# Kernel optimization log

Measured on AMD Instinct MI355X. Metric: run time of the kernel, lower is better.

The kernel has to match this reference:

```python
import jax, jax.numpy as jnp
import numpy as np
from functools import partial

B, H, W, C = 16, 64, 64, 512      # images, feature H, feature W, channels
R = 256                            # raw RPN proposals per image (sorted by objectness)
N_REGIONS = 64                     # regions kept after NMS
PH, PW = 7, 7                      # pool_size (h, w)
IOU_THR = 0.4
FH, FW = H, W                      # feature_size (h, w)
NEG = -jnp.inf


def _nms_indices(roi):
    # roi: [R, 4] (x, y, w, h). Scores are descending by construction
    # (tf.reverse(tf.range(n)/n)), so greedy NMS processes rows in order.
    x, y, w, h = roi[:, 0], roi[:, 1], roi[:, 2], roi[:, 3]
    y1, x1, y2, x2 = y, x, y + h, x + w
    area = (y2 - y1) * (x2 - x1)
    ih = jnp.maximum(jnp.minimum(y2[:, None], y2[None, :]) - jnp.maximum(y1[:, None], y1[None, :]), 0.0)
    iw = jnp.maximum(jnp.minimum(x2[:, None], x2[None, :]) - jnp.maximum(x1[:, None], x1[None, :]), 0.0)
    inter = ih * iw
    union = area[:, None] + area[None, :] - inter
    iou = jnp.where(union > 0, inter / union, 0.0)  # [R, R]

    def step(keep, xs):
        i, row = xs
        suppressed = jnp.any(keep & (row > IOU_THR))
        return keep.at[i].set(~suppressed), None

    keep, _ = jax.lax.scan(step, jnp.zeros((R,), bool), (jnp.arange(R), iou))
    rank = jnp.cumsum(keep.astype(jnp.int32)) - 1
    valid = keep & (rank < N_REGIONS)
    # Unfilled slot j gets tail index R - N_REGIONS + j, which is exactly
    # tf.concat([nms, tf.range(n_roi)[size(nms) - n_regions:]], 0).
    fill = R - N_REGIONS + jnp.arange(N_REGIONS)
    idx = fill.at[jnp.where(valid, rank, N_REGIONS)].set(jnp.arange(R), mode='drop')
    return idx


def _fix_axis(mn, mx, ps, fs):
    pad = ps - (mx - mn)
    fix_min = mn < pad // 2
    fix_max = fs - mx < (1 + pad) // 2
    symmetric = (pad > 0) & ~(fix_min | fix_max)
    omin = jnp.where(symmetric, mn - pad // 2, mn)
    omax = jnp.where(symmetric, mx + (1 + pad) // 2, mx)
    omin = jnp.where((pad > 0) & fix_min, 0, omin)
    omax = jnp.where((pad > 0) & fix_min, ps, omax)
    omin = jnp.where((pad > 0) & fix_max, fs - ps, omin)
    omax = jnp.where((pad > 0) & fix_max, fs, omax)
    return omin, omax


def _clip_roi(roi):
    # roi: [B, N_REGIONS, 4] float (x, y, w, h) -> int32 clipped (x, y, w, h)
    x_min = jnp.maximum(0.0, roi[..., 0]).astype(jnp.int32)
    y_min = jnp.maximum(0.0, roi[..., 1]).astype(jnp.int32)
    x_max = jnp.minimum(float(FW), roi[..., 0] + roi[..., 2]).astype(jnp.int32)
    y_max = jnp.minimum(float(FH), roi[..., 1] + roi[..., 3]).astype(jnp.int32)
    x_min, x_max = _fix_axis(x_min, x_max, PW, FW)   # x axis uses si=1 (width)
    y_min, y_max = _fix_axis(y_min, y_max, PH, FH)   # y axis uses si=0 (height)
    return jnp.stack([x_min, y_min, x_max - x_min, y_max - y_min], axis=-1)


def _pool_one(fm, r):
    # fm: [H, W, C]; r: int32 (x, y, w, h).
    # Faithful to the traced tf.function behaviour of _pool_roi: region.shape[0]
    # is dynamic (None) so region_shape = pool_size, hence h_step = w_step = 1:
    # bins i < PH-1 are single rows y+i; the last bin spans rows [y+PH-1, y+h).
    x, y, w, h = r[0], r[1], r[2], r[3]
    ii = y + jnp.arange(PH - 1)
    jj = x + jnp.arange(PW - 1)
    rmask = (jnp.arange(H) >= y + PH - 1) & (jnp.arange(H) < y + h)
    cmask = (jnp.arange(W) >= x + PW - 1) & (jnp.arange(W) < x + w)
    block = fm[ii[:, None], jj[None, :], :]                                   # [PH-1, PW-1, C]
    col_strip = jnp.max(jnp.where(cmask[None, :, None], fm, NEG), axis=1)     # [H, C]
    corner = jnp.max(jnp.where(rmask[:, None], col_strip, NEG), axis=0)       # [C]
    row_strip = jnp.max(jnp.where(rmask[:, None, None], fm[:, jj, :], NEG), axis=0)  # [PW-1, C]
    top = jnp.concatenate([block, col_strip[ii][:, None, :]], axis=1)         # [PH-1, PW, C]
    bottom = jnp.concatenate([row_strip, corner[None, :]], axis=0)[None]      # [1, PW, C]
    return jnp.concatenate([top, bottom], axis=0)                             # [PH, PW, C]


def _forward(features, roi):
    idx = jax.vmap(_nms_indices)(roi)                           # [B, N_REGIONS]
    roi_nms = jnp.take_along_axis(roi, idx[..., None], axis=1)  # [B, N_REGIONS, 4]
    roi_clipped = _clip_roi(roi_nms)                            # int32 [B, N_REGIONS, 4]
    pooled = jax.vmap(lambda fm, rs: jax.vmap(partial(_pool_one, fm))(rs))(features, roi_clipped)
    return pooled, roi_clipped


def setup_inputs():
    key = jax.random.key(0)
    k1, k2, k3 = jax.random.split(key, 3)
    features = jax.random.normal(k1, (B, H, W, C), dtype=jnp.float32)
    xy = jax.random.uniform(k2, (B, R, 2), dtype=jnp.float32) * 60.0
    wh = jax.random.uniform(k3, (B, R, 2), dtype=jnp.float32) * 30.0 + 2.0
    roi = jnp.concatenate([xy, wh], axis=-1)
    return {"features": features, "roi": roi}


def reference(features, roi):
    return _forward(features, roi)
```

## Files before the change

kernel.cpp:

```cpp
#include <hip/hip_runtime.h>
#include <math.h>

namespace {
constexpr int kB = 16, kH = 64, kW = 64, kC = 512;
constexpr int kR = 256, kN = 64, kPH = 7, kPW = 7;
constexpr int kC4 = kC / 4;
constexpr float kIouThr = 0.4f;
constexpr size_t kPooledElems = (size_t)kB * kN * kPH * kPW * kC;
}

__device__ __forceinline__ float4 max4(float4 a, float4 b) {
    return make_float4(fmaxf(a.x, b.x), fmaxf(a.y, b.y),
                       fmaxf(a.z, b.z), fmaxf(a.w, b.w));
}

__global__ __launch_bounds__(256) void nms_clip_kernel(
        const float* __restrict__ roi, float* __restrict__ out_roi) {
    const int b = blockIdx.x;
    const int tid = threadIdx.x;
    const float* r = roi + (size_t)b * kR * 4;

    __shared__ float4 box[kR];
    __shared__ float area[kR];
    __shared__ unsigned long long M[kR][4];
    __shared__ unsigned long long kw[4];
    __shared__ int idx[kN];

    if (tid < kN) idx[tid] = kR - kN + tid;

    const float4 rr = ((const float4*)r)[tid];
    const float x1 = rr.x, y1 = rr.y, x2 = rr.x + rr.z, y2 = rr.y + rr.w;
    box[tid] = make_float4(x1, y1, x2, y2);
    area[tid] = (y2 - y1) * (x2 - x1);
    __syncthreads();

    {
        unsigned long long m0 = 0, m1 = 0, m2 = 0, m3 = 0;
        const float ai = area[tid];
        for (int j = 0; j < kR; ++j) {
            const float4 bj = box[j];
            const float ih = fmaxf(fminf(y2, bj.w) - fmaxf(y1, bj.y), 0.0f);
            const float iw = fmaxf(fminf(x2, bj.z) - fmaxf(x1, bj.x), 0.0f);
            const float inter = ih * iw;
            const float uni = ai + area[j] - inter;
            const float iou = (uni > 0.0f) ? (inter / uni) : 0.0f;
            if (iou > kIouThr) {
                const unsigned long long bit = 1ull << (j & 63);
                if ((j >> 6) == 0) m0 |= bit;
                else if ((j >> 6) == 1) m1 |= bit;
                else if ((j >> 6) == 2) m2 |= bit;
                else m3 |= bit;
            }
        }
        M[tid][0] = m0; M[tid][1] = m1; M[tid][2] = m2; M[tid][3] = m3;
    }
    __syncthreads();

    if (tid == 0) {
        unsigned long long s0 = 0, s1 = 0, s2 = 0, s3 = 0;
        unsigned long long k0 = 0, k1 = 0, k2 = 0, k3 = 0;
        unsigned long long n0 = M[0][0], n1 = M[0][1], n2 = M[0][2], n3 = M[0][3];
#pragma unroll
        for (int wi = 0; wi < 4; ++wi) {
            for (int bi = 0; bi < 64; ++bi) {
                const unsigned long long m0 = n0, m1 = n1, m2 = n2, m3 = n3;
                const int ip = (wi * 64 + bi + 1) & 255;
                n0 = M[ip][0]; n1 = M[ip][1]; n2 = M[ip][2]; n3 = M[ip][3];
                const unsigned long long sw =
                    (wi == 0) ? s0 : (wi == 1) ? s1 : (wi == 2) ? s2 : s3;
                if (!((sw >> bi) & 1ull)) {
                    const unsigned long long bit = 1ull << bi;
                    if (wi == 0) k0 |= bit;
                    else if (wi == 1) k1 |= bit;
                    else if (wi == 2) k2 |= bit;
                    else k3 |= bit;
                    s0 |= m0; s1 |= m1; s2 |= m2; s3 |= m3;
                }
            }
        }
        kw[0] = k0; kw[1] = k1; kw[2] = k2; kw[3] = k3;
    }
    __syncthreads();

    {
        const int wi = tid >> 6, bi = tid & 63;
        const unsigned long long kwv = kw[wi];
        if ((kwv >> bi) & 1ull) {
            int rank = 0;
            for (int w2 = 0; w2 < wi; ++w2) rank += __popcll(kw[w2]);
            const unsigned long long below =
                (bi == 0) ? 0ull : (~0ull >> (64 - bi));
            rank += __popcll(kwv & below);
            if (rank < kN) idx[rank] = tid;
        }
    }
    __syncthreads();

    if (tid < kN) {
        const int i = idx[tid];
        const float x = r[i * 4 + 0], y = r[i * 4 + 1];
        const float w = r[i * 4 + 2], h = r[i * 4 + 3];
        int x_min = (int)fmaxf(0.0f, x);
        int y_min = (int)fmaxf(0.0f, y);
        int x_max = (int)fminf((float)kW, x + w);
        int y_max = (int)fminf((float)kH, y + h);
        {
            const int pad = kPW - (x_max - x_min);
            const bool fmn = x_min < (pad >> 1);
            const bool fmx = (kW - x_max) < ((1 + pad) >> 1);
            const bool sym = (pad > 0) && !(fmn || fmx);
            int omin = sym ? (x_min - (pad >> 1)) : x_min;
            int omax = sym ? (x_max + ((1 + pad) >> 1)) : x_max;
            if ((pad > 0) && fmn) { omin = 0; omax = kPW; }
            if ((pad > 0) && fmx) { omin = kW - kPW; omax = kW; }
            x_min = omin; x_max = omax;
        }
        {
            const int pad = kPH - (y_max - y_min);
            const bool fmn = y_min < (pad >> 1);
            const bool fmx = (kH - y_max) < ((1 + pad) >> 1);
            const bool sym = (pad > 0) && !(fmn || fmx);
            int omin = sym ? (y_min - (pad >> 1)) : y_min;
            int omax = sym ? (y_max + ((1 + pad) >> 1)) : y_max;
            if ((pad > 0) && fmn) { omin = 0; omax = kPH; }
            if ((pad > 0) && fmx) { omin = kH - kPH; omax = kH; }
            y_min = omin; y_max = omax;
        }
        float4 rf;
        rf.x = (float)x_min; rf.y = (float)y_min;
        rf.z = (float)(x_max - x_min); rf.w = (float)(y_max - y_min);
        ((float4*)out_roi)[b * kN + tid] = rf;
    }
}

__global__ __launch_bounds__(512) void pool_kernel(
        const float4* __restrict__ fm4, const float4* __restrict__ rcf,
        float4* __restrict__ out4) {
    const int rid = blockIdx.x;
    const int b = rid >> 6;
    const int tid = threadIdx.x;
    const int s = tid >> 7;
    const int t = tid & 127;
    const float4 rf = rcf[rid];
    const int x = (int)rf.x, y = (int)rf.y;
    const int w = (int)rf.z, h = (int)rf.w;

    const float4* fm = fm4 + (size_t)b * kH * kW * kC4;
    float4* out = out4 + (size_t)rid * (kPH * kPW) * kC4;

    const float NI = -__builtin_inff();
    const float4 ninf = make_float4(NI, NI, NI, NI);

    for (int p = s; p < 6; p += 4) {
        const float4* row = fm + (size_t)(y + p) * kW * kC4 + t;
#pragma unroll
        for (int q = 0; q < 6; ++q) {
            out[(p * 7 + q) * kC4 + t] = row[(size_t)(x + q) * kC4];
        }
        float4 m = ninf;
        for (int j = x + 6; j < x + w; ++j) {
            m = max4(m, row[(size_t)j * kC4]);
        }
        out[(p * 7 + 6) * kC4 + t] = m;
    }

    float4 pm[7];
#pragma unroll
    for (int o = 0; o < 7; ++o) pm[o] = ninf;
    for (int i = y + 6 + s; i < y + h; i += 4) {
        const float4* row = fm + (size_t)i * kW * kC4 + t;
#pragma unroll
        for (int q = 0; q < 6; ++q) {
            pm[q] = max4(pm[q], row[(size_t)(x + q) * kC4]);
        }
        float4 c = pm[6];
        for (int j = x + 6; j < x + w; ++j) {
            c = max4(c, row[(size_t)j * kC4]);
        }
        pm[6] = c;
    }

    __shared__ float4 red[3][7][128];
    if (s > 0) {
#pragma unroll
        for (int o = 0; o < 7; ++o) red[s - 1][o][t] = pm[o];
    }
    __syncthreads();
    if (s == 0) {
#pragma unroll
        for (int o = 0; o < 7; ++o) {
            float4 v = pm[o];
            v = max4(v, red[0][o][t]);
            v = max4(v, red[1][o][t]);
            v = max4(v, red[2][o][t]);
            out[(42 + o) * kC4 + t] = v;
        }
    }
}

extern "C" void kernel_launch(void* const* d_in, const int* in_sizes, int n_in,
                              void* d_out, int out_size, void* d_ws, size_t ws_size,
                              hipStream_t stream) {
    (void)in_sizes; (void)n_in; (void)d_ws; (void)ws_size; (void)out_size;
    const float* features = (const float*)d_in[0];
    const float* roi = (const float*)d_in[1];
    float* out = (float*)d_out;
    float* out_roi = out + kPooledElems;

    nms_clip_kernel<<<kB, 256, 0, stream>>>(roi, out_roi);
    pool_kernel<<<kB * kN, 512, 0, stream>>>(
        (const float4*)features, (const float4*)out_roi, (float4*)out);
}
```

Before: 346.5 us.

## Split pooling across channel halves, use nontemporal stores, and skip suppressed boxes in NMS

The pooling kernel now launches twice as many 256-thread blocks, each handling half of the channels for one region. Block order is interleaved so that consecutive blocks come from different images. Output writes use nontemporal stores to reduce cache pollution, and the cross-wave reduction becomes a two-stage tree. The serial greedy NMS scan now jumps straight to the next unsuppressed box with ffs instead of testing all 256 bits, which shortens the single-thread critical path at the cost of dependent shared-memory loads.

```diff
diff --git a/kernel.cpp b/kernel.cpp
--- a/kernel.cpp
+++ b/kernel.cpp
@@ -9,9 +9,16 @@
 constexpr size_t kPooledElems = (size_t)kB * kN * kPH * kPW * kC;
 }
 
+typedef float vfloat4 __attribute__((ext_vector_type(4)));
+
 __device__ __forceinline__ float4 max4(float4 a, float4 b) {
     return make_float4(fmaxf(a.x, b.x), fmaxf(a.y, b.y),
                        fmaxf(a.z, b.z), fmaxf(a.w, b.w));
+}
+
+__device__ __forceinline__ void nt_store4(float4* p, float4 v) {
+    vfloat4 nv = { v.x, v.y, v.z, v.w };
+    __builtin_nontemporal_store(nv, (vfloat4*)p);
 }
 
 __global__ __launch_bounds__(256) void nms_clip_kernel(
@@ -59,23 +66,21 @@
     if (tid == 0) {
         unsigned long long s0 = 0, s1 = 0, s2 = 0, s3 = 0;
         unsigned long long k0 = 0, k1 = 0, k2 = 0, k3 = 0;
-        unsigned long long n0 = M[0][0], n1 = M[0][1], n2 = M[0][2], n3 = M[0][3];
 #pragma unroll
         for (int wi = 0; wi < 4; ++wi) {
-            for (int bi = 0; bi < 64; ++bi) {
-                const unsigned long long m0 = n0, m1 = n1, m2 = n2, m3 = n3;
-                const int ip = (wi * 64 + bi + 1) & 255;
-                n0 = M[ip][0]; n1 = M[ip][1]; n2 = M[ip][2]; n3 = M[ip][3];
-                const unsigned long long sw =
-                    (wi == 0) ? s0 : (wi == 1) ? s1 : (wi == 2) ? s2 : s3;
-                if (!((sw >> bi) & 1ull)) {
-                    const unsigned long long bit = 1ull << bi;
-                    if (wi == 0) k0 |= bit;
-                    else if (wi == 1) k1 |= bit;
-                    else if (wi == 2) k2 |= bit;
-                    else k3 |= bit;
-                    s0 |= m0; s1 |= m1; s2 |= m2; s3 |= m3;
-                }
+            unsigned long long* sw =
+                (wi == 0) ? &s0 : (wi == 1) ? &s1 : (wi == 2) ? &s2 : &s3;
+            unsigned long long avail = ~(*sw);
+            while (avail) {
+                const int bi = __ffsll(avail) - 1;
+                const int i = wi * 64 + bi;
+                const unsigned long long bit = 1ull << bi;
+                if (wi == 0) k0 |= bit;
+                else if (wi == 1) k1 |= bit;
+                else if (wi == 2) k2 |= bit;
+                else k3 |= bit;
+                s0 |= M[i][0]; s1 |= M[i][1]; s2 |= M[i][2]; s3 |= M[i][3];
+                avail = ~(*sw) & ~((bit << 1) - 1);
             }
         }
         kw[0] = k0; kw[1] = k1; kw[2] = k2; kw[3] = k3;
@@ -133,14 +138,20 @@
     }
 }
 
-__global__ __launch_bounds__(512) void pool_kernel(
+__global__ __launch_bounds__(256) void pool_kernel(
         const float4* __restrict__ fm4, const float4* __restrict__ rcf,
         float4* __restrict__ out4) {
-    const int rid = blockIdx.x;
-    const int b = rid >> 6;
+    const int bid = blockIdx.x;
+    const int b = bid & 15;
+    const int rest = bid >> 4;
+    const int n = rest & 63;
+    const int ch = rest >> 6;
+    const int rid = b * 64 + n;
     const int tid = threadIdx.x;
-    const int s = tid >> 7;
-    const int t = tid & 127;
+    const int s = tid >> 6;
+    const int t = tid & 63;
+    const int c = ch * 64 + t;
+
     const float4 rf = rcf[rid];
     const int x = (int)rf.x, y = (int)rf.y;
     const int w = (int)rf.z, h = (int)rf.w;
@@ -152,48 +163,55 @@
     const float4 ninf = make_float4(NI, NI, NI, NI);
 
     for (int p = s; p < 6; p += 4) {
-        const float4* row = fm + (size_t)(y + p) * kW * kC4 + t;
+        const float4* row = fm + (size_t)(y + p) * kW * kC4 + c;
 #pragma unroll
         for (int q = 0; q < 6; ++q) {
-            out[(p * 7 + q) * kC4 + t] = row[(size_t)(x + q) * kC4];
+            nt_store4(&out[(p * 7 + q) * kC4 + c], row[(size_t)(x + q) * kC4]);
         }
         float4 m = ninf;
         for (int j = x + 6; j < x + w; ++j) {
             m = max4(m, row[(size_t)j * kC4]);
         }
-        out[(p * 7 + 6) * kC4 + t] = m;
+        nt_store4(&out[(p * 7 + 6) * kC4 + c], m);
     }
 
     float4 pm[7];
 #pragma unroll
     for (int o = 0; o < 7; ++o) pm[o] = ninf;
     for (int i = y + 6 + s; i < y + h; i += 4) {
-        const float4* row = fm + (size_t)i * kW * kC4 + t;
+        const float4* row = fm + (size_t)i * kW * kC4 + c;
 #pragma unroll
         for (int q = 0; q < 6; ++q) {
             pm[q] = max4(pm[q], row[(size_t)(x + q) * kC4]);
         }
-        float4 c = pm[6];
+        float4 cmax = pm[6];
         for (int j = x + 6; j < x + w; ++j) {
-            c = max4(c, row[(size_t)j * kC4]);
-        }
-        pm[6] = c;
-    }
-
-    __shared__ float4 red[3][7][128];
-    if (s > 0) {
-#pragma unroll
-        for (int o = 0; o < 7; ++o) red[s - 1][o][t] = pm[o];
+            cmax = max4(cmax, row[(size_t)j * kC4]);
+        }
+        pm[6] = cmax;
+    }
+
+    __shared__ float4 red[2][7][64];
+    if (s >= 2) {
+#pragma unroll
+        for (int o = 0; o < 7; ++o) red[s - 2][o][t] = pm[o];
+    }
+    __syncthreads();
+    if (s < 2) {
+#pragma unroll
+        for (int o = 0; o < 7; ++o) pm[o] = max4(pm[o], red[s][o][t]);
+    }
+    __syncthreads();
+    if (s == 1) {
+#pragma unroll
+        for (int o = 0; o < 7; ++o) red[0][o][t] = pm[o];
     }
     __syncthreads();
     if (s == 0) {
 #pragma unroll
         for (int o = 0; o < 7; ++o) {
-            float4 v = pm[o];
-            v = max4(v, red[0][o][t]);
-            v = max4(v, red[1][o][t]);
-            v = max4(v, red[2][o][t]);
-            out[(42 + o) * kC4 + t] = v;
+            const float4 v = max4(pm[o], red[0][o][t]);
+            nt_store4(&out[(42 + o) * kC4 + c], v);
         }
     }
 }
@@ -208,6 +226,6 @@
     float* out_roi = out + kPooledElems;
 
     nms_clip_kernel<<<kB, 256, 0, stream>>>(roi, out_roi);
-    pool_kernel<<<kB * kN, 512, 0, stream>>>(
+    pool_kernel<<<kB * kN * 2, 256, 0, stream>>>(
         (const float4*)features, (const float4*)out_roi, (float4*)out);
 }
```

After: 350.0 us. No clear change (+1.0%).
